# Performance work log

Hardware: AMD Instinct MI355X
Metric: run time of the kernel (lower is better)

## Reference

```python
import jax, jax.numpy as jnp
import numpy as np
from jax import lax
from functools import partial

TAU = 2.0
V_TH = 1.0
ATAN_ALPHA = 2.0
BN_EPS = 1e-5

# Heaviside spike with ATan surrogate gradient (spikingjelly surrogate.ATan, alpha=2)
@jax.custom_vjp
def atan_spike(x):
    return (x >= 0).astype(x.dtype)

def _atan_fwd(x):
    return atan_spike(x), x

def _atan_bwd(x, g):
    # d/dx ~ alpha/2 / (1 + (pi/2 * alpha * x)^2)
    s = (jnp.pi / 2.0) * ATAN_ALPHA * x
    return (g * (ATAN_ALPHA / 2.0) / (1.0 + s * s),)

atan_spike.defvjp(_atan_fwd, _atan_bwd)

def lif_multistep(x_seq):
    # x_seq: [T, B, ...]; LIFNode: decay_input=True, v_reset=0 (hard reset), v0=0
    def step(v, x):
        v = v + (x - v) / TAU           # charge with input decay
        s = atan_spike(v - V_TH)        # fire
        v = v * (1.0 - s)               # hard reset to 0 (reset not detached)
        return v, s
    v0 = jnp.zeros_like(x_seq[0])
    _, s_seq = lax.scan(step, v0, x_seq)
    return s_seq

def conv2d_seq(x_seq, w):
    # x_seq: [T, B, C, H, W] -> flatten T into batch for the conv
    T, B, C, H, W = x_seq.shape
    x = x_seq.reshape(T * B, C, H, W)
    y = lax.conv_general_dilated(x, w, window_strides=(1, 1),
                                 padding=[(1, 1), (1, 1)],
                                 dimension_numbers=('NCHW', 'OIHW', 'NCHW'))
    return y.reshape(T, B, w.shape[0], H, W)

def batchnorm_seq(x_seq, gamma, beta):
    # training-mode BN: stats over merged (T*B, H, W) per channel
    mean = jnp.mean(x_seq, axis=(0, 1, 3, 4), keepdims=True)
    var = jnp.var(x_seq, axis=(0, 1, 3, 4), keepdims=True)
    xhat = (x_seq - mean) * lax.rsqrt(var + BN_EPS)
    return xhat * gamma[None, None, :, None, None] + beta[None, None, :, None, None]

def avgpool2_seq(x_seq):
    T, B, C, H, W = x_seq.shape
    x = x_seq.reshape(T * B, C, H, W)
    y = lax.reduce_window(x, 0.0, lax.add, (1, 1, 2, 2), (1, 1, 2, 2), 'VALID') * 0.25
    return y.reshape(T, B, C, H // 2, W // 2)


def setup_inputs() -> dict:
    key = jax.random.key(0)
    ks = jax.random.split(key, 6)
    T, B = 8, 128
    return {
        'x_seq': jax.random.uniform(ks[0], (T, B, 3, 32, 32), jnp.float32),
        'conv1_w': jax.random.normal(ks[1], (64, 3, 3, 3), jnp.float32) * (1.0 / np.sqrt(3 * 9)),
        'bn1_g': jnp.ones((64,), jnp.float32),
        'bn1_b': jnp.zeros((64,), jnp.float32),
        'conv2_w': jax.random.normal(ks[2], (128, 64, 3, 3), jnp.float32) * (1.0 / np.sqrt(64 * 9)),
        'bn2_g': jnp.ones((128,), jnp.float32),
        'bn2_b': jnp.zeros((128,), jnp.float32),
        'fc1_w': jax.random.normal(ks[3], (256, 8192), jnp.float32) * (1.0 / np.sqrt(8192)),
        'fc2_w': jax.random.normal(ks[4], (10, 256), jnp.float32) * (1.0 / np.sqrt(256)),
        'fc2_b': jnp.zeros((10,), jnp.float32),
    }


def reference(x_seq, conv1_w, bn1_g, bn1_b, conv2_w, bn2_g, bn2_b, fc1_w, fc2_w, fc2_b):
    x = avgpool2_seq(lif_multistep(batchnorm_seq(conv2d_seq(x_seq, conv1_w), bn1_g, bn1_b)))
    x = avgpool2_seq(lif_multistep(batchnorm_seq(conv2d_seq(x, conv2_w), bn2_g, bn2_b)))
    T, B = x.shape[0], x.shape[1]
    x = x.reshape(T, B, -1)                                  # [T, B, 8192]
    x = lif_multistep(jnp.einsum('tbi,oi->tbo', x, fc1_w))   # [T, B, 256]
    logits_seq = jnp.einsum('tbi,oi->tbo', x, fc2_w) + fc2_b # [T, B, 10]
    return logits_seq
```

## Files before the change

kernel.cpp:

```cpp
#include <hip/hip_runtime.h>


#define LIF_STEP(vv, xx, ss) do { \
    vv = fmaf((xx) - vv, 0.5f, vv); \
    ss = (vv >= 1.0f) ? 1.0f : 0.0f; \
    vv = (vv >= 1.0f) ? 0.0f : vv; \
  } while (0)

typedef __attribute__((ext_vector_type(8))) short short8;
typedef __attribute__((ext_vector_type(4))) float f32x4;

__device__ __forceinline__ float bf2f(unsigned short u) {
  return __uint_as_float(((unsigned)u) << 16);
}
__device__ __forceinline__ unsigned short f2bf(float f) {
  return (unsigned short)(__float_as_uint(f) >> 16);
}

#define OFF_POOL1   0u
#define OFF_POOL2   8388608u
#define OFF_PRE     12582912u
#define OFF_STATS   46137344u
#define OFF_FC1S    46162304u
#define OFF_A2      46424448u
#define OFF_B1      46535040u
#define OFF_A1      49680768u
#define ZERO_STATS 24576u

__global__ __launch_bounds__(256) void zero_kernel(float* __restrict__ p, unsigned n) {
  unsigned i = blockIdx.x * 256u + threadIdx.x;
  if (i < n) p[i] = 0.0f;
}

__global__ __launch_bounds__(256) void prep_w1(const float* __restrict__ w, unsigned short* __restrict__ A1) {
  int i = blockIdx.x * 256 + threadIdx.x;
  if (i >= 2048) return;
  int co = i >> 5, k = i & 31;
  float wv = 0.f;
  if (k < 27) {
    int tap = k / 3, ci = k - tap * 3;
    wv = w[co * 27 + ci * 9 + tap];
  }
  unsigned short hi = f2bf(wv);
  float rem = wv - bf2f(hi);
  unsigned short lo = f2bf(rem);
  float rem2 = rem - bf2f(lo);
  A1[i] = hi;
  A1[2048 + i] = lo;
  A1[4096 + i] = f2bf(rem2);
}

__global__ __launch_bounds__(256) void prep_w2(const float* __restrict__ w, unsigned short* __restrict__ A2) {
  int i = blockIdx.x * 256 + threadIdx.x;
  if (i >= 73728) return;
  int co = i / 576, r = i - co * 576;
  int ci = r / 9, t9 = r - ci * 9;
  int k = t9 * 64 + ci;
  int kc = k >> 5, q = (k >> 3) & 3, j = k & 7;
  int off = ((kc * 128 + co) * 4 + q) * 8 + j;
  float wv = w[i];
  unsigned short hi = f2bf(wv);
  float rem = wv - bf2f(hi);
  unsigned short lo = f2bf(rem);
  float rem2 = rem - bf2f(lo);
  A2[off] = hi;
  A2[73728 + off] = lo;
  A2[147456 + off] = f2bf(rem2);
}

__global__ __launch_bounds__(256) void prep_b1(const float* __restrict__ w, unsigned short* __restrict__ B1) {
  __shared__ unsigned short sh[2][8192];
  int blk = blockIdx.x;
  int sv = blk >> 7, opair = blk & 127;
  int tid = threadIdx.x;
  for (int o_l = 0; o_l < 2; ++o_l) {
    for (int it = 0; it < 32; ++it) {
      int korig = tid + 256 * it;
      float wv = w[(size_t)(opair * 2 + o_l) * 8192 + korig];
      unsigned short hi = f2bf(wv);
      float rem = wv - bf2f(hi);
      unsigned short lo = f2bf(rem);
      unsigned short pc = (sv == 0) ? hi : (sv == 1) ? lo : f2bf(rem - bf2f(lo));
      int k = (korig & 63) * 128 + (korig >> 6);
      sh[o_l][k] = pc;
    }
  }
  __syncthreads();
  unsigned short* outp = B1 + (size_t)sv * 2097152;
  for (int it = 0; it < 64; ++it) {
    int idx = tid + 256 * it;
    int kc = idx >> 6, r = idx & 63;
    int o_l = r >> 5, m = r & 31;
    outp[kc * 8192 + opair * 64 + r] = sh[o_l][kc * 32 + m];
  }
}

__global__ void finalize_bn1(const float* __restrict__ s1p,
                             const float* __restrict__ g, const float* __restrict__ b,
                             float* __restrict__ scale, float* __restrict__ shift, float inv_n) {
  int c = threadIdx.x;
  float s1 = 0.f, s2 = 0.f;
#pragma unroll 8
  for (int sp = 0; sp < 64; ++sp) {
    s1 += s1p[sp * 128 + c];
    s2 += s1p[sp * 128 + 64 + c];
  }
  float mean = s1 * inv_n;
  float var = fmaxf(s2 * inv_n - mean * mean, 0.0f);
  float rstd = rsqrtf(var + 1e-5f);
  float sc = g[c] * rstd;
  scale[c] = sc;
  shift[c] = fmaf(-mean, sc, b[c]);
}

__global__ void finalize_bn2(const float* __restrict__ s2p,
                             const float* __restrict__ g, const float* __restrict__ b,
                             float* __restrict__ scale, float* __restrict__ shift, float inv_n) {
  int c = threadIdx.x;
  float s1 = 0.f, s2 = 0.f;
#pragma unroll 8
  for (int sp = 0; sp < 64; ++sp) {
    s1 += s2p[sp * 256 + c];
    s2 += s2p[sp * 256 + 128 + c];
  }
  float mean = s1 * inv_n;
  float var = fmaxf(s2 * inv_n - mean * mean, 0.0f);
  float rstd = rsqrtf(var + 1e-5f);
  float sc = g[c] * rstd;
  scale[c] = sc;
  shift[c] = fmaf(-mean, sc, b[c]);
}

__global__ __launch_bounds__(256) void conv1_pass1_mfma(const float* __restrict__ x,
    const unsigned short* __restrict__ A1, float* __restrict__ s1p) {
  int b = blockIdx.x >> 3, yq = blockIdx.x & 7;
  int y0 = yq * 4;
  int sp = blockIdx.x & 63;
  int tid = threadIdx.x, wave = tid >> 6, lane = tid & 63;
  int xl = lane & 15, q = lane >> 4;
  __shared__ float xs[648];
  short8 A[3][4];
#pragma unroll
  for (int mt = 0; mt < 4; ++mt) {
    int aoff = (mt * 16 + xl) * 32 + q * 8;
    A[0][mt] = *(const short8*)(A1 + aoff);
    A[1][mt] = *(const short8*)(A1 + 2048 + aoff);
    A[2][mt] = *(const short8*)(A1 + 4096 + aoff);
  }
  int cb[8]; bool vld[8];
#pragma unroll
  for (int j = 0; j < 8; ++j) {
    int k = q * 8 + j;
    int tap = k / 3, ci = k - tap * 3;
    int dy = tap / 3, dx = tap - dy * 3;
    vld[j] = (k < 27);
    cb[j] = ci * 216 + (wave + dy) * 36 + dx + xl;
  }
  float s1[4][4], s2[4][4];
#pragma unroll
  for (int mt = 0; mt < 4; ++mt)
#pragma unroll
    for (int reg = 0; reg < 4; ++reg) { s1[mt][reg] = 0.f; s2[mt][reg] = 0.f; }

#pragma unroll 1
  for (int t = 0; t < 8; ++t) {
    int tb = t * 128 + b;
    const float* xb = x + tb * 3072;
    __syncthreads();
    for (int i = tid; i < 648; i += 256) {
      int ci = i / 216, r1 = i - ci * 216;
      int rr = r1 / 36, c = r1 - rr * 36;
      int gy = y0 - 1 + rr, gx = c - 1;
      xs[i] = ((unsigned)gy < 32u && (unsigned)gx < 32u) ? xb[(ci * 32 + gy) * 32 + gx] : 0.f;
    }
    __syncthreads();
    f32x4 acc[2][4];
#pragma unroll
    for (int tile = 0; tile < 2; ++tile)
#pragma unroll
      for (int mt = 0; mt < 4; ++mt) acc[tile][mt] = (f32x4){0.f, 0.f, 0.f, 0.f};
#pragma unroll
    for (int tile = 0; tile < 2; ++tile) {
      short8 Bh = (short8){0,0,0,0,0,0,0,0};
      short8 Bl = (short8){0,0,0,0,0,0,0,0};
      short8 Bll = (short8){0,0,0,0,0,0,0,0};
#pragma unroll
      for (int j = 0; j < 8; ++j) {
        float xv = vld[j] ? xs[cb[j] + tile * 16] : 0.f;
        unsigned short h = f2bf(xv);
        float r = xv - bf2f(h);
        unsigned short l = f2bf(r);
        float r2 = r - bf2f(l);
        Bh[j] = (short)h; Bl[j] = (short)l; Bll[j] = (short)f2bf(r2);
      }
#pragma unroll
      for (int mt = 0; mt < 4; ++mt) {
        f32x4 a = acc[tile][mt];
        a = __builtin_amdgcn_mfma_f32_16x16x32_bf16(A[0][mt], Bh, a, 0, 0, 0);
        a = __builtin_amdgcn_mfma_f32_16x16x32_bf16(A[1][mt], Bh, a, 0, 0, 0);
        a = __builtin_amdgcn_mfma_f32_16x16x32_bf16(A[2][mt], Bh, a, 0, 0, 0);
        a = __builtin_amdgcn_mfma_f32_16x16x32_bf16(A[0][mt], Bl, a, 0, 0, 0);
        a = __builtin_amdgcn_mfma_f32_16x16x32_bf16(A[1][mt], Bl, a, 0, 0, 0);
        a = __builtin_amdgcn_mfma_f32_16x16x32_bf16(A[2][mt], Bl, a, 0, 0, 0);
        a = __builtin_amdgcn_mfma_f32_16x16x32_bf16(A[0][mt], Bll, a, 0, 0, 0);
        a = __builtin_amdgcn_mfma_f32_16x16x32_bf16(A[1][mt], Bll, a, 0, 0, 0);
        acc[tile][mt] = a;
      }
    }
#pragma unroll
    for (int tile = 0; tile < 2; ++tile)
#pragma unroll
      for (int mt = 0; mt < 4; ++mt)
#pragma unroll
        for (int reg = 0; reg < 4; ++reg) {
          float val = acc[tile][mt][reg];
          s1[mt][reg] += val; s2[mt][reg] = fmaf(val, val, s2[mt][reg]);
        }
  }
#pragma unroll
  for (int mt = 0; mt < 4; ++mt)
#pragma unroll
    for (int reg = 0; reg < 4; ++reg) {
      float a1 = s1[mt][reg], a2 = s2[mt][reg];
#pragma unroll
      for (int off = 1; off < 16; off <<= 1) { a1 += __shfl_xor(a1, off); a2 += __shfl_xor(a2, off); }
      if (xl == 0) {
        int co = mt * 16 + q * 4 + reg;
        atomicAdd(&s1p[sp * 128 + co], a1);
        atomicAdd(&s1p[sp * 128 + 64 + co], a2);
      }
    }
}

__global__ __launch_bounds__(256) void conv1_fused_mfma(const float* __restrict__ x,
    const unsigned short* __restrict__ A1, const float* __restrict__ scale,
    const float* __restrict__ shift, unsigned short* __restrict__ pool1) {
  int b = blockIdx.x >> 3, yq = blockIdx.x & 7;
  int y0 = yq * 4;
  int tid = threadIdx.x, wave = tid >> 6, lane = tid & 63;
  int xl = lane & 15, q = lane >> 4;
  __shared__ float xs[648];
  __shared__ unsigned short shout[4 * 16 * 72];
  short8 A[3][4];
#pragma unroll
  for (int mt = 0; mt < 4; ++mt) {
    int aoff = (mt * 16 + xl) * 32 + q * 8;
    A[0][mt] = *(const short8*)(A1 + aoff);
    A[1][mt] = *(const short8*)(A1 + 2048 + aoff);
    A[2][mt] = *(const short8*)(A1 + 4096 + aoff);
  }
  int cb[8]; bool vld[8];
#pragma unroll
  for (int j = 0; j < 8; ++j) {
    int k = q * 8 + j;
    int tap = k / 3, ci = k - tap * 3;
    int dy = tap / 3, dx = tap - dy * 3;
    vld[j] = (k < 27);
    cb[j] = ci * 216 + (wave + dy) * 36 + dx + xl;
  }
  float scr[4][4], shr[4][4];
#pragma unroll
  for (int mt = 0; mt < 4; ++mt)
#pragma unroll
    for (int reg = 0; reg < 4; ++reg) {
      int co = mt * 16 + q * 4 + reg;
      scr[mt][reg] = scale[co]; shr[mt][reg] = shift[co];
    }
  float v[2][4][4];
#pragma unroll
  for (int tile = 0; tile < 2; ++tile)
#pragma unroll
    for (int mt = 0; mt < 4; ++mt)
#pragma unroll
      for (int reg = 0; reg < 4; ++reg) v[tile][mt][reg] = 0.f;

#pragma unroll 1
  for (int t = 0; t < 8; ++t) {
    int tb = t * 128 + b;
    const float* xb = x + tb * 3072;
    __syncthreads();
    for (int i = tid; i < 648; i += 256) {
      int ci = i / 216, r1 = i - ci * 216;
      int rr = r1 / 36, c = r1 - rr * 36;
      int gy = y0 - 1 + rr, gx = c - 1;
      xs[i] = ((unsigned)gy < 32u && (unsigned)gx < 32u) ? xb[(ci * 32 + gy) * 32 + gx] : 0.f;
    }
    __syncthreads();
    f32x4 acc[2][4];
#pragma unroll
    for (int tile = 0; tile < 2; ++tile)
#pragma unroll
      for (int mt = 0; mt < 4; ++mt) acc[tile][mt] = (f32x4){0.f, 0.f, 0.f, 0.f};
#pragma unroll
    for (int tile = 0; tile < 2; ++tile) {
      short8 Bh = (short8){0,0,0,0,0,0,0,0};
      short8 Bl = (short8){0,0,0,0,0,0,0,0};
      short8 Bll = (short8){0,0,0,0,0,0,0,0};
#pragma unroll
      for (int j = 0; j < 8; ++j) {
        float xv = vld[j] ? xs[cb[j] + tile * 16] : 0.f;
        unsigned short h = f2bf(xv);
        float r = xv - bf2f(h);
        unsigned short l = f2bf(r);
        float r2 = r - bf2f(l);
        Bh[j] = (short)h; Bl[j] = (short)l; Bll[j] = (short)f2bf(r2);
      }
#pragma unroll
      for (int mt = 0; mt < 4; ++mt) {
        f32x4 a = acc[tile][mt];
        a = __builtin_amdgcn_mfma_f32_16x16x32_bf16(A[0][mt], Bh, a, 0, 0, 0);
        a = __builtin_amdgcn_mfma_f32_16x16x32_bf16(A[1][mt], Bh, a, 0, 0, 0);
        a = __builtin_amdgcn_mfma_f32_16x16x32_bf16(A[2][mt], Bh, a, 0, 0, 0);
        a = __builtin_amdgcn_mfma_f32_16x16x32_bf16(A[0][mt], Bl, a, 0, 0, 0);
        a = __builtin_amdgcn_mfma_f32_16x16x32_bf16(A[1][mt], Bl, a, 0, 0, 0);
        a = __builtin_amdgcn_mfma_f32_16x16x32_bf16(A[2][mt], Bl, a, 0, 0, 0);
        a = __builtin_amdgcn_mfma_f32_16x16x32_bf16(A[0][mt], Bll, a, 0, 0, 0);
        a = __builtin_amdgcn_mfma_f32_16x16x32_bf16(A[1][mt], Bll, a, 0, 0, 0);
        acc[tile][mt] = a;
      }
    }
#pragma unroll
    for (int mt = 0; mt < 4; ++mt)
#pragma unroll
      for (int rp = 0; rp < 2; ++rp) {
        float hp[2][2];
#pragma unroll
        for (int tile = 0; tile < 2; ++tile)
#pragma unroll
          for (int e = 0; e < 2; ++e) {
            int reg = rp * 2 + e;
            float xv = fmaf(acc[tile][mt][reg], scr[mt][reg], shr[mt][reg]);
            float spk;
            LIF_STEP(v[tile][mt][reg], xv, spk);
            hp[tile][e] = spk + __shfl_xor(spk, 1);
          }
        int tw = xl & 1;
        float h0 = tw ? hp[1][0] : hp[0][0];
        float h1 = tw ? hp[1][1] : hp[0][1];
        unsigned u = (unsigned)f2bf(h0) | ((unsigned)f2bf(h1) << 16);
        int pp = tw * 8 + (xl >> 1);
        *(unsigned*)&shout[(wave * 16 + pp) * 72 + mt * 16 + q * 4 + rp * 2] = u;
      }
    __syncthreads();
    {
      int cg = tid >> 5, py_l = (tid >> 4) & 1, px = tid & 15;
      uint4 ua = *(const uint4*)&shout[((2 * py_l) * 16 + px) * 72 + cg * 8];
      uint4 ub = *(const uint4*)&shout[((2 * py_l + 1) * 16 + px) * 72 + cg * 8];
      const unsigned* pa = (const unsigned*)&ua;
      const unsigned* pb = (const unsigned*)&ub;
      unsigned o[4];
#pragma unroll
      for (int e = 0; e < 4; ++e) {
        float a0 = bf2f((unsigned short)(pa[e] & 0xffffu)), a1 = bf2f((unsigned short)(pa[e] >> 16));
        float b0 = bf2f((unsigned short)(pb[e] & 0xffffu)), b1 = bf2f((unsigned short)(pb[e] >> 16));
        o[e] = (unsigned)f2bf(0.25f * (a0 + b0)) | ((unsigned)f2bf(0.25f * (a1 + b1)) << 16);
      }
      int py = yq * 2 + py_l;
      *(uint4*)(pool1 + (size_t)tb * 16384 + cg * 2048 + (py * 16 + px) * 8) =
          make_uint4(o[0], o[1], o[2], o[3]);
    }
  }
}

__device__ __forceinline__ void c2_load_a(const unsigned short* __restrict__ A2, int kc,
                                          int m0, int xl, int q, short8 (&a)[2][3]) {
#pragma unroll
  for (int mt = 0; mt < 2; ++mt) {
    int aoff = ((kc * 128 + m0 + mt * 16 + xl) * 4 + q) * 8;
    a[mt][0] = *(const short8*)(A2 + aoff);
    a[mt][1] = *(const short8*)(A2 + 73728 + aoff);
    a[mt][2] = *(const short8*)(A2 + 147456 + aoff);
  }
}
__device__ __forceinline__ void c2_step8(const unsigned short* __restrict__ simg, int kc,
                                         int xl, int q, short8 (&a)[2][3], f32x4 (&acc)[2][8]) {
  int tap = kc >> 1;
  int dy = tap / 3, dx = tap - dy * 3;
  int cgq = (kc & 1) * 4 + q;
#pragma unroll
  for (int yl = 0; yl < 8; ++yl) {
    int baddr = (((yl + dy) * 8 + cgq) * 18 + (xl + dx)) * 8;
    short8 bb = *(const short8*)(simg + baddr);
#pragma unroll
    for (int mt = 0; mt < 2; ++mt) {
      acc[mt][yl] = __builtin_amdgcn_mfma_f32_16x16x32_bf16(a[mt][0], bb, acc[mt][yl], 0, 0, 0);
      acc[mt][yl] = __builtin_amdgcn_mfma_f32_16x16x32_bf16(a[mt][1], bb, acc[mt][yl], 0, 0, 0);
      acc[mt][yl] = __builtin_amdgcn_mfma_f32_16x16x32_bf16(a[mt][2], bb, acc[mt][yl], 0, 0, 0);
    }
  }
}

__global__ __launch_bounds__(256, 2) void conv2_store_mfma(const unsigned short* __restrict__ pool1,
    const unsigned short* __restrict__ A2, float* __restrict__ preact, float* __restrict__ s2p) {
  int bx = blockIdx.x;
  int tb = bx >> 1, half = bx & 1;
  int sp = bx & 63;
  __shared__ unsigned short simg[10 * 8 * 18 * 8];
  int tid = threadIdx.x;
  const unsigned* src = (const unsigned*)(pool1 + (size_t)tb * 16384);
  unsigned* dstw = (unsigned*)simg;
  for (int i = tid; i < 5760; i += 256) {
    int cp = i & 3, rest = i >> 2;
    int jj = rest / 18, xx = rest - jj * 18;
    int cg = jj & 7, row_l = jj >> 3;
    int yi = half * 8 - 1 + row_l, gx = xx - 1;
    unsigned val = 0u;
    if ((unsigned)yi < 16u && (unsigned)gx < 16u)
      val = src[cg * 1024 + yi * 64 + gx * 4 + cp];
    dstw[i] = val;
  }
  __syncthreads();

  int wave = tid >> 6, lane = tid & 63;
  int xl = lane & 15, q = lane >> 4;
  int m0 = wave * 32;
  f32x4 acc[2][8];
#pragma unroll
  for (int mt = 0; mt < 2; ++mt)
#pragma unroll
    for (int yl = 0; yl < 8; ++yl) acc[mt][yl] = (f32x4){0.f, 0.f, 0.f, 0.f};

  short8 aA[2][3], aB[2][3];
  c2_load_a(A2, 0, m0, xl, q, aA);
#pragma unroll 1
  for (int kc = 0; kc < 18; kc += 2) {
    c2_load_a(A2, kc + 1, m0, xl, q, aB);
    c2_step8(simg, kc, xl, q, aA, acc);
    if (kc + 2 < 18) c2_load_a(A2, kc + 2, m0, xl, q, aA);
    c2_step8(simg, kc + 1, xl, q, aB, acc);
  }

  float* pre = preact + (size_t)tb * 32768;
#pragma unroll
  for (int mt = 0; mt < 2; ++mt)
#pragma unroll
    for (int reg = 0; reg < 4; ++reg) {
      int co = m0 + mt * 16 + q * 4 + reg;
      float s1 = 0.f, s2 = 0.f;
#pragma unroll
      for (int yl = 0; yl < 8; ++yl) {
        float val = acc[mt][yl][reg];
        int row = half * 8 + yl;
        pre[(row * 128 + co) * 16 + xl] = val;
        s1 += val; s2 = fmaf(val, val, s2);
      }
#pragma unroll
      for (int off = 1; off < 16; off <<= 1) {
        s1 += __shfl_xor(s1, off); s2 += __shfl_xor(s2, off);
      }
      if (xl == 0) {
        atomicAdd(&s2p[sp * 256 + co], s1);
        atomicAdd(&s2p[sp * 256 + 128 + co], s2);
      }
    }
}

__global__ __launch_bounds__(256) void bn2_lif_pool(const float* __restrict__ pre,
    const float* __restrict__ scale, const float* __restrict__ shift,
    unsigned short* __restrict__ pool2) {
  int b = blockIdx.x >> 3, py = blockIdx.x & 7;
  int tid = threadIdx.x;
  int co = tid >> 1, half = tid & 1;
  __shared__ unsigned short shout[8 * 136];
  float sc = scale[co], sh = shift[co];
  float v[4][4];
#pragma unroll
  for (int p = 0; p < 4; ++p)
#pragma unroll
    for (int e = 0; e < 4; ++e) v[p][e] = 0.f;

#pragma unroll 1
  for (int t = 0; t < 8; ++t) {
    const float* base = pre + ((size_t)((t * 128 + b) * 16 + 2 * py)) * 2048 + co * 16 + half * 8;
    __syncthreads();
    float4 r0a = *(const float4*)(base);
    float4 r0b = *(const float4*)(base + 4);
    float4 r1a = *(const float4*)(base + 2048);
    float4 r1b = *(const float4*)(base + 2048 + 4);
    float p00[4] = {r0a.x, r0a.z, r0b.x, r0b.z};
    float p01[4] = {r0a.y, r0a.w, r0b.y, r0b.w};
    float p10[4] = {r1a.x, r1a.z, r1b.x, r1b.z};
    float p11[4] = {r1a.y, r1a.w, r1b.y, r1b.w};
#pragma unroll
    for (int p = 0; p < 4; ++p) {
      float s00, s01, s10, s11, xv;
      xv = fmaf(p00[p], sc, sh); LIF_STEP(v[p][0], xv, s00);
      xv = fmaf(p01[p], sc, sh); LIF_STEP(v[p][1], xv, s01);
      xv = fmaf(p10[p], sc, sh); LIF_STEP(v[p][2], xv, s10);
      xv = fmaf(p11[p], sc, sh); LIF_STEP(v[p][3], xv, s11);
      shout[(half * 4 + p) * 136 + co] = f2bf(0.25f * (s00 + s01 + s10 + s11));
    }
    __syncthreads();
    {
      int s_l = tid >> 5, ci4 = (tid & 31) * 4;
      uint2 vv = *(const uint2*)&shout[s_l * 136 + ci4];
      *(uint2*)(pool2 + ((size_t)(t * 128 + b) * 64 + py * 8 + s_l) * 128 + ci4) = vv;
    }
  }
}

__global__ __launch_bounds__(256, 2) void fc1_mfma(const unsigned short* __restrict__ pool2,
    const unsigned short* __restrict__ B1, float* __restrict__ partial) {
  int bx = blockIdx.x;
  int t_o = bx & 1, tbt = (bx >> 1) & 15, kb = bx >> 5;
  int tid = threadIdx.x, wave = tid >> 6, lane = tid & 63;
  int xl = lane & 15, q = lane >> 4;
  int m0 = t_o * 128 + wave * 32;
  int n0 = tbt * 64;
  __shared__ unsigned short sB[2][64 * 42];
  f32x4 acc[2][4];
#pragma unroll
  for (int mt = 0; mt < 2; ++mt)
#pragma unroll
    for (int nt = 0; nt < 4; ++nt) acc[mt][nt] = (f32x4){0.f, 0.f, 0.f, 0.f};

#pragma unroll 1
  for (int kc0 = 0; kc0 < 16; kc0 += 2) {
    int kc = kb * 16 + kc0;
    __syncthreads();
    {
      int tb_l = tid >> 2, kq = tid & 3;
      const unsigned short* srcp = pool2 + (size_t)(n0 + tb_l) * 8192 + kc * 32 + kq * 8;
      uint4 v0 = *(const uint4*)(srcp);
      uint4 v1 = *(const uint4*)(srcp + 32);
      *(uint4*)(sB[0] + tb_l * 42 + kq * 8) = v0;
      *(uint4*)(sB[1] + tb_l * 42 + kq * 8) = v1;
    }
    __syncthreads();
#pragma unroll
    for (int sub = 0; sub < 2; ++sub) {
      int kcs = kc + sub;
      short8 a[2][3];
#pragma unroll
      for (int mt = 0; mt < 2; ++mt) {
        int aoff = ((kcs * 256 + m0 + mt * 16 + xl) * 4 + q) * 8;
        a[mt][0] = *(const short8*)(B1 + aoff);
        a[mt][1] = *(const short8*)(B1 + 2097152 + aoff);
        a[mt][2] = *(const short8*)(B1 + 4194304 + aoff);
      }
#pragma unroll
      for (int nt = 0; nt < 4; ++nt) {
        short8 bb = *(const short8*)(sB[sub] + (nt * 16 + xl) * 42 + q * 8);
#pragma unroll
        for (int mt = 0; mt < 2; ++mt) {
          acc[mt][nt] = __builtin_amdgcn_mfma_f32_16x16x32_bf16(a[mt][0], bb, acc[mt][nt], 0, 0, 0);
          acc[mt][nt] = __builtin_amdgcn_mfma_f32_16x16x32_bf16(a[mt][1], bb, acc[mt][nt], 0, 0, 0);
          acc[mt][nt] = __builtin_amdgcn_mfma_f32_16x16x32_bf16(a[mt][2], bb, acc[mt][nt], 0, 0, 0);
        }
      }
    }
  }
#pragma unroll
  for (int mt = 0; mt < 2; ++mt)
#pragma unroll
    for (int nt = 0; nt < 4; ++nt)
#pragma unroll
      for (int reg = 0; reg < 4; ++reg) {
        int o = m0 + mt * 16 + q * 4 + reg;
        partial[((size_t)kb * 256 + o) * 1024 + n0 + nt * 16 + xl] = acc[mt][nt][reg];
      }
}

__global__ __launch_bounds__(256) void reduce_lif(const float* __restrict__ partial, float* __restrict__ fs) {
  int idx = blockIdx.x * 256 + threadIdx.x;
  int o = idx >> 7, b = idx & 127;
  float v = 0.f;
#pragma unroll 1
  for (int t = 0; t < 8; ++t) {
    float xv = 0.f;
#pragma unroll
    for (int kb = 0; kb < 16; ++kb)
      xv += partial[((size_t)kb * 256 + o) * 1024 + t * 128 + b];
    float s;
    LIF_STEP(v, xv, s);
    fs[t * 32768 + b * 256 + o] = s;
  }
}

__global__ __launch_bounds__(256) void fc2_kernel(const float* __restrict__ fs, const float* __restrict__ w,
                                                  const float* __restrict__ bias, float* __restrict__ outp) {
  int tb = blockIdx.x;
  __shared__ float sv[256];
  int tid = threadIdx.x;
  sv[tid] = fs[tb * 256 + tid];
  __syncthreads();
  if (tid < 10) {
    float a = bias[tid];
    const float* wr = w + tid * 256;
#pragma unroll 8
    for (int o = 0; o < 256; ++o) a = fmaf(sv[o], wr[o], a);
    outp[tb * 10 + tid] = a;
  }
}

extern "C" void kernel_launch(void* const* d_in, const int* in_sizes, int n_in,
                              void* d_out, int out_size, void* d_ws, size_t ws_size,
                              hipStream_t stream) {
  (void)in_sizes; (void)n_in; (void)out_size; (void)ws_size;
  const float* x_seq   = (const float*)d_in[0];
  const float* conv1_w = (const float*)d_in[1];
  const float* bn1_g   = (const float*)d_in[2];
  const float* bn1_b   = (const float*)d_in[3];
  const float* conv2_w = (const float*)d_in[4];
  const float* bn2_g   = (const float*)d_in[5];
  const float* bn2_b   = (const float*)d_in[6];
  const float* fc1_w   = (const float*)d_in[7];
  const float* fc2_w   = (const float*)d_in[8];
  const float* fc2_b   = (const float*)d_in[9];
  float* out = (float*)d_out;
  float* ws  = (float*)d_ws;

  unsigned short* pool1 = (unsigned short*)(ws + OFF_POOL1);
  float* fc1_part = ws + OFF_POOL1;
  unsigned short* pool2 = (unsigned short*)(ws + OFF_POOL2);
  float* preact  = ws + OFF_PRE;
  float* fc1_s   = ws + OFF_FC1S;
  unsigned short* A2 = (unsigned short*)(ws + OFF_A2);
  unsigned short* B1 = (unsigned short*)(ws + OFF_B1);
  unsigned short* A1 = (unsigned short*)(ws + OFF_A1);
  float* st      = ws + OFF_STATS;
  float* s1p    = st;
  float* s2p    = st + 8192;
  float* bn1_sc = st + 24576;  float* bn1_sh = st + 24640;
  float* bn2_sc = st + 24704;  float* bn2_sh = st + 24832;

  zero_kernel<<<96, 256, 0, stream>>>(st, ZERO_STATS);
  prep_w1<<<8, 256, 0, stream>>>(conv1_w, A1);
  prep_w2<<<288, 256, 0, stream>>>(conv2_w, A2);
  prep_b1<<<384, 256, 0, stream>>>(fc1_w, B1);
  conv1_pass1_mfma<<<1024, 256, 0, stream>>>(x_seq, A1, s1p);
  finalize_bn1<<<1, 64, 0, stream>>>(s1p, bn1_g, bn1_b, bn1_sc, bn1_sh, 1.0f / 1048576.0f);
  conv1_fused_mfma<<<1024, 256, 0, stream>>>(x_seq, A1, bn1_sc, bn1_sh, pool1);
  conv2_store_mfma<<<2048, 256, 0, stream>>>(pool1, A2, preact, s2p);
  finalize_bn2<<<1, 128, 0, stream>>>(s2p, bn2_g, bn2_b, bn2_sc, bn2_sh, 1.0f / 262144.0f);
  bn2_lif_pool<<<1024, 256, 0, stream>>>(preact, bn2_sc, bn2_sh, pool2);
  fc1_mfma<<<512, 256, 0, stream>>>(pool2, B1, fc1_part);
  reduce_lif<<<128, 256, 0, stream>>>(fc1_part, fc1_s);
  fc2_kernel<<<1024, 256, 0, stream>>>(fc1_s, fc2_w, fc2_b, out);
}
```

Measured before the change: 362.7 us.

## Merge prep kernels and fold BN finalize and fc2 into neighbouring kernels

Merges the zeroing and three weight-prep kernels into one launch, computes the BN scale and shift inside each consumer block instead of in separate single-block finalize kernels, and fuses the fc1 reduce+LIF with fc2 through LDS. The goal is fewer kernel launches and less serialization on tiny kernels, from 13 launches down to 7. In exchange every consumer block redundantly reads and reduces the 64 stat partials, and the fc2 stage now runs on only 128 blocks.

```diff
diff --git a/kernel.cpp b/kernel.cpp
--- a/kernel.cpp
+++ b/kernel.cpp
@@ -27,108 +27,74 @@
 #define OFF_A1      49680768u
 #define ZERO_STATS 24576u
 
-__global__ __launch_bounds__(256) void zero_kernel(float* __restrict__ p, unsigned n) {
-  unsigned i = blockIdx.x * 256u + threadIdx.x;
-  if (i < n) p[i] = 0.0f;
-}
-
-__global__ __launch_bounds__(256) void prep_w1(const float* __restrict__ w, unsigned short* __restrict__ A1) {
-  int i = blockIdx.x * 256 + threadIdx.x;
-  if (i >= 2048) return;
-  int co = i >> 5, k = i & 31;
-  float wv = 0.f;
-  if (k < 27) {
-    int tap = k / 3, ci = k - tap * 3;
-    wv = w[co * 27 + ci * 9 + tap];
-  }
-  unsigned short hi = f2bf(wv);
-  float rem = wv - bf2f(hi);
-  unsigned short lo = f2bf(rem);
-  float rem2 = rem - bf2f(lo);
-  A1[i] = hi;
-  A1[2048 + i] = lo;
-  A1[4096 + i] = f2bf(rem2);
-}
-
-__global__ __launch_bounds__(256) void prep_w2(const float* __restrict__ w, unsigned short* __restrict__ A2) {
-  int i = blockIdx.x * 256 + threadIdx.x;
-  if (i >= 73728) return;
-  int co = i / 576, r = i - co * 576;
-  int ci = r / 9, t9 = r - ci * 9;
-  int k = t9 * 64 + ci;
-  int kc = k >> 5, q = (k >> 3) & 3, j = k & 7;
-  int off = ((kc * 128 + co) * 4 + q) * 8 + j;
-  float wv = w[i];
-  unsigned short hi = f2bf(wv);
-  float rem = wv - bf2f(hi);
-  unsigned short lo = f2bf(rem);
-  float rem2 = rem - bf2f(lo);
-  A2[off] = hi;
-  A2[73728 + off] = lo;
-  A2[147456 + off] = f2bf(rem2);
-}
-
-__global__ __launch_bounds__(256) void prep_b1(const float* __restrict__ w, unsigned short* __restrict__ B1) {
-  __shared__ unsigned short sh[2][8192];
-  int blk = blockIdx.x;
-  int sv = blk >> 7, opair = blk & 127;
+__global__ __launch_bounds__(256) void prep_all(const float* __restrict__ w1,
+    const float* __restrict__ w2, const float* __restrict__ wfc1,
+    float* __restrict__ st, unsigned short* __restrict__ A1,
+    unsigned short* __restrict__ A2, unsigned short* __restrict__ B1) {
+  int bx = blockIdx.x;
   int tid = threadIdx.x;
-  for (int o_l = 0; o_l < 2; ++o_l) {
-    for (int it = 0; it < 32; ++it) {
-      int korig = tid + 256 * it;
-      float wv = w[(size_t)(opair * 2 + o_l) * 8192 + korig];
+  if (bx < 96) {
+    unsigned i = bx * 256u + tid;
+    if (i < ZERO_STATS) st[i] = 0.0f;
+  } else if (bx < 104) {
+    int i = (bx - 96) * 256 + tid;
+    if (i < 2048) {
+      int co = i >> 5, k = i & 31;
+      float wv = 0.f;
+      if (k < 27) {
+        int tap = k / 3, ci = k - tap * 3;
+        wv = w1[co * 27 + ci * 9 + tap];
+      }
       unsigned short hi = f2bf(wv);
       float rem = wv - bf2f(hi);
       unsigned short lo = f2bf(rem);
-      unsigned short pc = (sv == 0) ? hi : (sv == 1) ? lo : f2bf(rem - bf2f(lo));
-      int k = (korig & 63) * 128 + (korig >> 6);
-      sh[o_l][k] = pc;
-    }
-  }
-  __syncthreads();
-  unsigned short* outp = B1 + (size_t)sv * 2097152;
-  for (int it = 0; it < 64; ++it) {
-    int idx = tid + 256 * it;
-    int kc = idx >> 6, r = idx & 63;
-    int o_l = r >> 5, m = r & 31;
-    outp[kc * 8192 + opair * 64 + r] = sh[o_l][kc * 32 + m];
-  }
-}
-
-__global__ void finalize_bn1(const float* __restrict__ s1p,
-                             const float* __restrict__ g, const float* __restrict__ b,
-                             float* __restrict__ scale, float* __restrict__ shift, float inv_n) {
-  int c = threadIdx.x;
-  float s1 = 0.f, s2 = 0.f;
-#pragma unroll 8
-  for (int sp = 0; sp < 64; ++sp) {
-    s1 += s1p[sp * 128 + c];
-    s2 += s1p[sp * 128 + 64 + c];
-  }
-  float mean = s1 * inv_n;
-  float var = fmaxf(s2 * inv_n - mean * mean, 0.0f);
-  float rstd = rsqrtf(var + 1e-5f);
-  float sc = g[c] * rstd;
-  scale[c] = sc;
-  shift[c] = fmaf(-mean, sc, b[c]);
-}
-
-__global__ void finalize_bn2(const float* __restrict__ s2p,
-                             const float* __restrict__ g, const float* __restrict__ b,
-                             float* __restrict__ scale, float* __restrict__ shift, float inv_n) {
-  int c = threadIdx.x;
-  float s1 = 0.f, s2 = 0.f;
-#pragma unroll 8
-  for (int sp = 0; sp < 64; ++sp) {
-    s1 += s2p[sp * 256 + c];
-    s2 += s2p[sp * 256 + 128 + c];
-  }
-  float mean = s1 * inv_n;
-  float var = fmaxf(s2 * inv_n - mean * mean, 0.0f);
-  float rstd = rsqrtf(var + 1e-5f);
-  float sc = g[c] * rstd;
-  scale[c] = sc;
-  shift[c] = fmaf(-mean, sc, b[c]);
+      float rem2 = rem - bf2f(lo);
+      A1[i] = hi;
+      A1[2048 + i] = lo;
+      A1[4096 + i] = f2bf(rem2);
+    }
+  } else if (bx < 392) {
+    int i = (bx - 104) * 256 + tid;
+    if (i < 73728) {
+      int co = i / 576, r = i - co * 576;
+      int ci = r / 9, t9 = r - ci * 9;
+      int k = t9 * 64 + ci;
+      int kc = k >> 5, q = (k >> 3) & 3, j = k & 7;
+      int off = ((kc * 128 + co) * 4 + q) * 8 + j;
+      float wv = w2[i];
+      unsigned short hi = f2bf(wv);
+      float rem = wv - bf2f(hi);
+      unsigned short lo = f2bf(rem);
+      float rem2 = rem - bf2f(lo);
+      A2[off] = hi;
+      A2[73728 + off] = lo;
+      A2[147456 + off] = f2bf(rem2);
+    }
+  } else {
+    __shared__ unsigned short sh[2][8192];
+    int blk = bx - 392;
+    int sv = blk >> 7, opair = blk & 127;
+    for (int o_l = 0; o_l < 2; ++o_l) {
+      for (int it = 0; it < 32; ++it) {
+        int korig = tid + 256 * it;
+        float wv = wfc1[(size_t)(opair * 2 + o_l) * 8192 + korig];
+        unsigned short hi = f2bf(wv);
+        float rem = wv - bf2f(hi);
+        unsigned short lo = f2bf(rem);
+        unsigned short pc = (sv == 0) ? hi : (sv == 1) ? lo : f2bf(rem - bf2f(lo));
+        int k = (korig & 63) * 128 + (korig >> 6);
+        sh[o_l][k] = pc;
+      }
+    }
+    __syncthreads();
+    unsigned short* outp = B1 + (size_t)sv * 2097152;
+    for (int it = 0; it < 64; ++it) {
+      int idx = tid + 256 * it;
+      int kc = idx >> 6, r = idx & 63;
+      int o_l = r >> 5, m = r & 31;
+      outp[kc * 8192 + opair * 64 + r] = sh[o_l][kc * 32 + m];
+    }
+  }
 }
 
 __global__ __launch_bounds__(256) void conv1_pass1_mfma(const float* __restrict__ x,
@@ -233,14 +199,31 @@
 }
 
 __global__ __launch_bounds__(256) void conv1_fused_mfma(const float* __restrict__ x,
-    const unsigned short* __restrict__ A1, const float* __restrict__ scale,
-    const float* __restrict__ shift, unsigned short* __restrict__ pool1) {
+    const unsigned short* __restrict__ A1, const float* __restrict__ s1p,
+    const float* __restrict__ g, const float* __restrict__ bb_,
+    unsigned short* __restrict__ pool1) {
   int b = blockIdx.x >> 3, yq = blockIdx.x & 7;
   int y0 = yq * 4;
   int tid = threadIdx.x, wave = tid >> 6, lane = tid & 63;
   int xl = lane & 15, q = lane >> 4;
   __shared__ float xs[648];
   __shared__ unsigned short shout[4 * 16 * 72];
+  __shared__ float scsh[128];
+  if (tid < 64) {
+    int c = tid;
+    float t1 = 0.f, t2 = 0.f;
+#pragma unroll 8
+    for (int sp = 0; sp < 64; ++sp) {
+      t1 += s1p[sp * 128 + c];
+      t2 += s1p[sp * 128 + 64 + c];
+    }
+    float mean = t1 * (1.0f / 1048576.0f);
+    float var = fmaxf(t2 * (1.0f / 1048576.0f) - mean * mean, 0.0f);
+    float rstd = rsqrtf(var + 1e-5f);
+    float sc = g[c] * rstd;
+    scsh[c] = sc;
+    scsh[64 + c] = fmaf(-mean, sc, bb_[c]);
+  }
   short8 A[3][4];
 #pragma unroll
   for (int mt = 0; mt < 4; ++mt) {
@@ -258,13 +241,14 @@
     vld[j] = (k < 27);
     cb[j] = ci * 216 + (wave + dy) * 36 + dx + xl;
   }
+  __syncthreads();
   float scr[4][4], shr[4][4];
 #pragma unroll
   for (int mt = 0; mt < 4; ++mt)
 #pragma unroll
     for (int reg = 0; reg < 4; ++reg) {
       int co = mt * 16 + q * 4 + reg;
-      scr[mt][reg] = scale[co]; shr[mt][reg] = shift[co];
+      scr[mt][reg] = scsh[co]; shr[mt][reg] = scsh[64 + co];
     }
   float v[2][4][4];
 #pragma unroll
@@ -456,13 +440,30 @@
 }
 
 __global__ __launch_bounds__(256) void bn2_lif_pool(const float* __restrict__ pre,
-    const float* __restrict__ scale, const float* __restrict__ shift,
+    const float* __restrict__ s2p, const float* __restrict__ g, const float* __restrict__ bb_,
     unsigned short* __restrict__ pool2) {
   int b = blockIdx.x >> 3, py = blockIdx.x & 7;
   int tid = threadIdx.x;
   int co = tid >> 1, half = tid & 1;
   __shared__ unsigned short shout[8 * 136];
-  float sc = scale[co], sh = shift[co];
+  __shared__ float scsh[256];
+  if (tid < 128) {
+    int c = tid;
+    float t1 = 0.f, t2 = 0.f;
+#pragma unroll 8
+    for (int sp = 0; sp < 64; ++sp) {
+      t1 += s2p[sp * 256 + c];
+      t2 += s2p[sp * 256 + 128 + c];
+    }
+    float mean = t1 * (1.0f / 262144.0f);
+    float var = fmaxf(t2 * (1.0f / 262144.0f) - mean * mean, 0.0f);
+    float rstd = rsqrtf(var + 1e-5f);
+    float sc = g[c] * rstd;
+    scsh[c] = sc;
+    scsh[128 + c] = fmaf(-mean, sc, bb_[c]);
+  }
+  __syncthreads();
+  float sc = scsh[co], sh = scsh[128 + co];
   float v[4][4];
 #pragma unroll
   for (int p = 0; p < 4; ++p)
@@ -561,9 +562,11 @@
       }
 }
 
-__global__ __launch_bounds__(256) void reduce_lif(const float* __restrict__ partial, float* __restrict__ fs) {
-  int idx = blockIdx.x * 256 + threadIdx.x;
-  int o = idx >> 7, b = idx & 127;
+__global__ __launch_bounds__(256) void fc_tail(const float* __restrict__ partial,
+    const float* __restrict__ w2, const float* __restrict__ bias, float* __restrict__ outp) {
+  int b = blockIdx.x;
+  int o = threadIdx.x;
+  __shared__ float sp_lds[8 * 256];
   float v = 0.f;
 #pragma unroll 1
   for (int t = 0; t < 8; ++t) {
@@ -573,23 +576,17 @@
       xv += partial[((size_t)kb * 256 + o) * 1024 + t * 128 + b];
     float s;
     LIF_STEP(v, xv, s);
-    fs[t * 32768 + b * 256 + o] = s;
-  }
-}
-
-__global__ __launch_bounds__(256) void fc2_kernel(const float* __restrict__ fs, const float* __restrict__ w,
-                                                  const float* __restrict__ bias, float* __restrict__ outp) {
-  int tb = blockIdx.x;
-  __shared__ float sv[256];
-  int tid = threadIdx.x;
-  sv[tid] = fs[tb * 256 + tid];
+    sp_lds[t * 256 + o] = s;
+  }
   __syncthreads();
-  if (tid < 10) {
-    float a = bias[tid];
-    const float* wr = w + tid * 256;
+  if (threadIdx.x < 80) {
+    int t = threadIdx.x & 7, o10 = threadIdx.x >> 3;
+    float a = bias[o10];
+    const float* wr = w2 + o10 * 256;
+    const float* sv = sp_lds + t * 256;
 #pragma unroll 8
-    for (int o = 0; o < 256; ++o) a = fmaf(sv[o], wr[o], a);
-    outp[tb * 10 + tid] = a;
+    for (int k = 0; k < 256; ++k) a = fmaf(sv[k], wr[k], a);
+    outp[(t * 128 + b) * 10 + o10] = a;
   }
 }
 
@@ -614,27 +611,18 @@
   float* fc1_part = ws + OFF_POOL1;
   unsigned short* pool2 = (unsigned short*)(ws + OFF_POOL2);
   float* preact  = ws + OFF_PRE;
-  float* fc1_s   = ws + OFF_FC1S;
   unsigned short* A2 = (unsigned short*)(ws + OFF_A2);
   unsigned short* B1 = (unsigned short*)(ws + OFF_B1);
   unsigned short* A1 = (unsigned short*)(ws + OFF_A1);
   float* st      = ws + OFF_STATS;
   float* s1p    = st;
   float* s2p    = st + 8192;
-  float* bn1_sc = st + 24576;  float* bn1_sh = st + 24640;
-  float* bn2_sc = st + 24704;  float* bn2_sh = st + 24832;
-
-  zero_kernel<<<96, 256, 0, stream>>>(st, ZERO_STATS);
-  prep_w1<<<8, 256, 0, stream>>>(conv1_w, A1);
-  prep_w2<<<288, 256, 0, stream>>>(conv2_w, A2);
-  prep_b1<<<384, 256, 0, stream>>>(fc1_w, B1);
+
+  prep_all<<<776, 256, 0, stream>>>(conv1_w, conv2_w, fc1_w, st, A1, A2, B1);
   conv1_pass1_mfma<<<1024, 256, 0, stream>>>(x_seq, A1, s1p);
-  finalize_bn1<<<1, 64, 0, stream>>>(s1p, bn1_g, bn1_b, bn1_sc, bn1_sh, 1.0f / 1048576.0f);
-  conv1_fused_mfma<<<1024, 256, 0, stream>>>(x_seq, A1, bn1_sc, bn1_sh, pool1);
+  conv1_fused_mfma<<<1024, 256, 0, stream>>>(x_seq, A1, s1p, bn1_g, bn1_b, pool1);
   conv2_store_mfma<<<2048, 256, 0, stream>>>(pool1, A2, preact, s2p);
-  finalize_bn2<<<1, 128, 0, stream>>>(s2p, bn2_g, bn2_b, bn2_sc, bn2_sh, 1.0f / 262144.0f);
-  bn2_lif_pool<<<1024, 256, 0, stream>>>(preact, bn2_sc, bn2_sh, pool2);
+  bn2_lif_pool<<<1024, 256, 0, stream>>>(preact, s2p, bn2_g, bn2_b, pool2);
   fc1_mfma<<<512, 256, 0, stream>>>(pool2, B1, fc1_part);
-  reduce_lif<<<128, 256, 0, stream>>>(fc1_part, fc1_s);
-  fc2_kernel<<<1024, 256, 0, stream>>>(fc1_s, fc2_w, fc2_b, out);
-}
+  fc_tail<<<128, 256, 0, stream>>>(fc1_part, fc2_w, fc2_b, out);
+}
```

Result: slower. 381.9 us (+5.3%).
